# Optimization experiments

Hardware: AMD Instinct MI355X
Metric: run time of the kernel (lower is better)

## Reference

```python
import jax, jax.numpy as jnp
import numpy as np
import math

N, Tp1, V = 256, 33, 10000
D_FEAT, H, W_DIM = 1280, 512, 256
NULL_IDX = 0


def setup_inputs() -> dict:
    key = jax.random.key(0)
    ks = jax.random.split(key, 10)
    feats = jax.random.normal(ks[0], (N, D_FEAT, 4, 4), dtype=jnp.float32)
    captions = jax.random.randint(ks[1], (N, Tp1), 0, V)
    W_proj = jax.random.normal(ks[2], (D_FEAT, H), dtype=jnp.float32) / math.sqrt(D_FEAT)
    b_proj = jnp.zeros((H,), dtype=jnp.float32)
    W_embed = jax.random.normal(ks[3], (V, W_DIM), dtype=jnp.float32) / math.sqrt(V)
    Wx = jax.random.normal(ks[4], (W_DIM, 4 * H), dtype=jnp.float32) / math.sqrt(W_DIM)
    Wh = jax.random.normal(ks[5], (H, 4 * H), dtype=jnp.float32) / math.sqrt(H)
    Wattn = jax.random.normal(ks[6], (H, 4 * H), dtype=jnp.float32) / math.sqrt(H)
    b = jnp.zeros((4 * H,), dtype=jnp.float32)
    W_vocab = jax.random.normal(ks[7], (H, V), dtype=jnp.float32) / math.sqrt(H)
    b_vocab = jnp.zeros((V,), dtype=jnp.float32)
    return {"feats": feats, "captions": captions, "W_proj": W_proj, "b_proj": b_proj,
            "W_embed": W_embed, "Wx": Wx, "Wh": Wh, "Wattn": Wattn, "b": b,
            "W_vocab": W_vocab, "b_vocab": b_vocab}


def _attention_lstm(x, A_flat, h0, Wx, Wh, Wattn, b):
    # x: (N,T,W), A_flat: (N,H,16), h0: (N,H)
    Hh = h0.shape[1]
    scale = 1.0 / math.sqrt(Hh)

    def step(carry, x_t):
        h, c = carry
        # scaled dot-product attention over the 16 spatial positions
        scores = jnp.einsum('nh,nhp->np', h, A_flat) * scale       # (N,16)
        w = jax.nn.softmax(scores, axis=1)
        attn = jnp.einsum('nhp,np->nh', A_flat, w)                 # (N,H)
        a = x_t @ Wx + h @ Wh + b + attn @ Wattn                   # (N,4H)
        i = jax.nn.sigmoid(a[:, 0:Hh])
        f = jax.nn.sigmoid(a[:, Hh:2 * Hh])
        o = jax.nn.sigmoid(a[:, 2 * Hh:3 * Hh])
        g = jnp.tanh(a[:, 3 * Hh:4 * Hh])
        c_next = f * c + i * g
        h_next = o * jnp.tanh(c_next)
        return (h_next, c_next), h_next

    (_, _), hs = jax.lax.scan(step, (h0, h0), jnp.swapaxes(x, 0, 1))
    return jnp.swapaxes(hs, 0, 1)  # (N,T,H)


def reference(feats, captions, W_proj, b_proj, W_embed, Wx, Wh, Wattn, b, W_vocab, b_vocab):
    cap_in = captions[:, :-1]   # (N,T)
    cap_out = captions[:, 1:]   # (N,T)
    # project CNN features per spatial location: (N,Dfeat,4,4) -> (N,H,4,4)
    A = jnp.einsum('ncij,ch->nhij', feats, W_proj) + b_proj[None, :, None, None]
    h0 = A.mean(axis=(2, 3))                     # (N,H); c0 = h0
    A_flat = A.reshape(A.shape[0], A.shape[1], 16)
    x = W_embed[cap_in]                           # (N,T,W)
    h = _attention_lstm(x, A_flat, h0, Wx, Wh, Wattn, b)
    scores = jnp.einsum('nth,hv->ntv', h, W_vocab) + b_vocab   # (N,T,V)
    # temporal softmax loss, sum over tokens (ignoring NULL), averaged over N
    logp = jax.nn.log_softmax(scores, axis=-1)
    nll = -jnp.take_along_axis(logp, cap_out[..., None], axis=-1)[..., 0]  # (N,T)
    mask = (cap_out != NULL_IDX).astype(scores.dtype)
    loss = jnp.sum(nll * mask) / scores.shape[0]
    return loss
```

## Files before the change

### kernel.cpp

```cpp
#include <hip/hip_runtime.h>
#include <hip/hip_bf16.h>

#define NB   256
#define NT   32
#define NV   10000
#define NVP  10240
#define NDF  1280
#define NH   512
#define VT_N 40

typedef short bf16x8 __attribute__((ext_vector_type(8)));
typedef float f32x4  __attribute__((ext_vector_type(4)));
typedef unsigned short u16;

__device__ __forceinline__ float b2f(u16 u) {
    union { unsigned i; float f; } v; v.i = ((unsigned)u) << 16; return v.f;
}
__device__ __forceinline__ u16 f2b(float f) {
    union { float f; unsigned i; } v; v.f = f;
    unsigned r = v.i + 0x7FFF + ((v.i >> 16) & 1);
    return (u16)(r >> 16);
}

__device__ __forceinline__ void gload16(const u16* g, u16* l) {
    __builtin_amdgcn_global_load_lds(
        (const __attribute__((address_space(1))) void*)g,
        (__attribute__((address_space(3))) void*)l, 16, 0, 0);
}

static const size_t B_C     = 0;
static const size_t B_SCP   = B_C     + (size_t)256*512*4;
static const size_t B_PMAX  = B_SCP   + (size_t)2*32*256*16*4;
static const size_t B_PSUM  = B_PMAX  + (size_t)8192*VT_N*4;
static const size_t B_TGT   = B_PSUM  + (size_t)8192*VT_N*4;
static const size_t B_LOSS  = B_TGT   + (size_t)8192*4;
static const size_t B_AB    = B_LOSS  + 16;
static const size_t B_XPB   = B_AB    + (size_t)256*16*512*2;
static const size_t B_HALLB = B_XPB   + (size_t)32*256*2048*2;
static const size_t B_WVT   = B_HALLB + (size_t)32*256*512*2;
static const size_t B_WXT   = B_WVT   + (size_t)10240*512*2;
static const size_t B_WHAT  = B_WXT   + (size_t)2048*256*2;
static const size_t B_HB0   = B_WHAT  + (size_t)2048*1024*2;
static const size_t B_HB1   = B_HB0   + (size_t)256*512*2;
static const size_t B_PREAW = B_HB1   + (size_t)256*512*2;

__global__ __launch_bounds__(256) void tconv_kernel(
    const float* __restrict__ src, u16* __restrict__ dst,
    int K, int N, int Npad, int ldK, int koff)
{
    __shared__ u16 tile[64][65];
    const int k0 = blockIdx.y * 64, n0 = blockIdx.x * 64, tid = threadIdx.x;
#pragma unroll
    for (int i = 0; i < 16; i++) {
        int idx = tid + i * 256;
        int kk = idx >> 6, nn = idx & 63;
        int n = n0 + nn;
        float v = (n < N) ? src[(size_t)(k0 + kk) * N + n] : 0.f;
        tile[kk][nn] = f2b(v);
    }
    __syncthreads();
#pragma unroll
    for (int i = 0; i < 16; i++) {
        int idx = tid + i * 256;
        int nn = idx >> 6, kk = idx & 63;
        int n = n0 + nn;
        if (n < Npad) dst[(size_t)n * ldK + koff + k0 + kk] = tile[kk][nn];
    }
}

__global__ __launch_bounds__(256) void ftrans_kernel(
    const float* __restrict__ feats, u16* __restrict__ fT)
{
    const int cch = blockIdx.x, n = blockIdx.y, tid = threadIdx.x;
    __shared__ u16 lt[64][17];
    const int c0 = cch * 64;
    const int c = tid >> 2, p4 = (tid & 3) * 4;
    float4 v = *(const float4*)(feats + (size_t)n * 20480 + (size_t)(c0 + c) * 16 + p4);
    lt[c][p4] = f2b(v.x); lt[c][p4 + 1] = f2b(v.y);
    lt[c][p4 + 2] = f2b(v.z); lt[c][p4 + 3] = f2b(v.w);
    __syncthreads();
    const int p = tid >> 4, cg = tid & 15;
    ushort4 o;
    o.x = lt[cg * 4 + 0][p]; o.y = lt[cg * 4 + 1][p];
    o.z = lt[cg * 4 + 2][p]; o.w = lt[cg * 4 + 3][p];
    *(ushort4*)(fT + (size_t)(n * 16 + p) * 1280 + c0 + cg * 4) = o;
}

__global__ __launch_bounds__(256) void proj_gemm_kernel(
    const u16* __restrict__ fT, const u16* __restrict__ WpT,
    const float* __restrict__ bp, u16* __restrict__ Ab)
{
    const int ct = blockIdx.x, rt = blockIdx.y;
    const int tid = threadIdx.x, w = tid >> 6, lane = tid & 63;
    const int r0 = rt * 64;
    const int lm = lane & 15, lkq = lane >> 4, lk = lkq * 8;
    const int nbase = ct * 128 + w * 32;

    f32x4 acc[4][2];
#pragma unroll
    for (int mt = 0; mt < 4; mt++)
#pragma unroll
        for (int nt = 0; nt < 2; nt++) acc[mt][nt] = (f32x4){0.f, 0.f, 0.f, 0.f};

    for (int kc = 0; kc < 1280; kc += 32) {
        bf16x8 af[4];
#pragma unroll
        for (int mt = 0; mt < 4; mt++)
            af[mt] = *(const bf16x8*)(fT + (size_t)(r0 + mt * 16 + lm) * 1280 + kc + lk);
#pragma unroll
        for (int nt = 0; nt < 2; nt++) {
            bf16x8 bfg = *(const bf16x8*)(WpT + (size_t)(nbase + nt * 16 + lm) * 1280 + kc + lk);
#pragma unroll
            for (int mt = 0; mt < 4; mt++)
                acc[mt][nt] = __builtin_amdgcn_mfma_f32_16x16x32_bf16(af[mt], bfg, acc[mt][nt], 0, 0, 0);
        }
    }
    float bbv[2];
#pragma unroll
    for (int nt = 0; nt < 2; nt++) bbv[nt] = bp[nbase + nt * 16 + lm];
#pragma unroll
    for (int mt = 0; mt < 4; mt++)
#pragma unroll
        for (int nt = 0; nt < 2; nt++)
#pragma unroll
            for (int r = 0; r < 4; r++) {
                int row = r0 + mt * 16 + lkq * 4 + r;
                int col = nbase + nt * 16 + lm;
                Ab[(size_t)row * 512 + col] = f2b(acc[mt][nt][r] + bbv[nt]);
            }
}

__global__ __launch_bounds__(256) void projmean_kernel(
    const u16* __restrict__ Ab, float* __restrict__ c0, u16* __restrict__ hb0)
{
    const int n = blockIdx.x, tid = threadIdx.x;
    const int col0 = tid, col1 = tid + 256;
    float s0 = 0.f, s1 = 0.f;
#pragma unroll
    for (int p = 0; p < 16; p++) {
        const u16* ap = Ab + ((size_t)n * 16 + p) * 512;
        s0 += b2f(ap[col0]);
        s1 += b2f(ap[col1]);
    }
    s0 *= 0.0625f; s1 *= 0.0625f;
    c0[n * 512 + col0] = s0;  c0[n * 512 + col1] = s1;
    hb0[(size_t)n * 512 + col0] = f2b(s0);
    hb0[(size_t)n * 512 + col1] = f2b(s1);
}

__global__ __launch_bounds__(256) void xp_mfma_kernel(
    const int* __restrict__ caps, const float* __restrict__ We,
    const u16* __restrict__ Wxt, const float* __restrict__ bb,
    u16* __restrict__ xpb)
{
    const int ct = blockIdx.x, rt = blockIdx.y;
    const int tid = threadIdx.x, w = tid >> 6, lane = tid & 63;
    const int r0 = rt * 64;
    const int lm = lane & 15, lkq = lane >> 4, lk = lkq * 8;
    const int nbase = ct * 512 + w * 128;

    int capm[4];
#pragma unroll
    for (int mt = 0; mt < 4; mt++) {
        int row = r0 + mt * 16 + lm;
        capm[mt] = caps[(row >> 5) * 33 + (row & 31)];
    }
    f32x4 acc[4][8];
#pragma unroll
    for (int mt = 0; mt < 4; mt++)
#pragma unroll
        for (int nt = 0; nt < 8; nt++) acc[mt][nt] = (f32x4){0.f, 0.f, 0.f, 0.f};

    for (int kc = 0; kc < 256; kc += 32) {
        bf16x8 af[4];
#pragma unroll
        for (int mt = 0; mt < 4; mt++) {
            const float* ap = We + (size_t)capm[mt] * 256 + kc + lk;
            float4 f0 = *(const float4*)ap;
            float4 f1 = *(const float4*)(ap + 4);
            bf16x8 t;
            t[0] = (short)f2b(f0.x); t[1] = (short)f2b(f0.y);
            t[2] = (short)f2b(f0.z); t[3] = (short)f2b(f0.w);
            t[4] = (short)f2b(f1.x); t[5] = (short)f2b(f1.y);
            t[6] = (short)f2b(f1.z); t[7] = (short)f2b(f1.w);
            af[mt] = t;
        }
#pragma unroll
        for (int nt = 0; nt < 8; nt++) {
            bf16x8 bfg = *(const bf16x8*)(Wxt + (size_t)(nbase + nt * 16 + lm) * 256 + kc + lk);
#pragma unroll
            for (int mt = 0; mt < 4; mt++)
                acc[mt][nt] = __builtin_amdgcn_mfma_f32_16x16x32_bf16(af[mt], bfg, acc[mt][nt], 0, 0, 0);
        }
    }
    float bbv[8];
#pragma unroll
    for (int nt = 0; nt < 8; nt++) bbv[nt] = bb[nbase + nt * 16 + lm];
#pragma unroll
    for (int mt = 0; mt < 4; mt++)
#pragma unroll
        for (int nt = 0; nt < 8; nt++)
#pragma unroll
            for (int r = 0; r < 4; r++) {
                int row = r0 + mt * 16 + lkq * 4 + r;
                int col = nbase + nt * 16 + lm;
                float v = acc[mt][nt][r] + bbv[nt];
                xpb[((size_t)(row & 31) * 256 + (row >> 5)) * 2048 + col] = f2b(v);
            }
}

__global__ __launch_bounds__(256) void preaw_mfma_kernel(
    const u16* __restrict__ Ab, const u16* __restrict__ what,
    u16* __restrict__ preaw)
{
    const int ct = blockIdx.x, rt = blockIdx.y;
    const int tid = threadIdx.x, w = tid >> 6, lane = tid & 63;
    const int r0 = rt * 64;
    const int lm = lane & 15, lkq = lane >> 4, lk = lkq * 8;
    const int nbase = ct * 512 + w * 128;

    f32x4 acc[4][8];
#pragma unroll
    for (int mt = 0; mt < 4; mt++)
#pragma unroll
        for (int nt = 0; nt < 8; nt++) acc[mt][nt] = (f32x4){0.f, 0.f, 0.f, 0.f};

    for (int kc = 0; kc < 512; kc += 32) {
        bf16x8 af[4];
#pragma unroll
        for (int mt = 0; mt < 4; mt++)
            af[mt] = *(const bf16x8*)(Ab + (size_t)(r0 + mt * 16 + lm) * 512 + kc + lk);
#pragma unroll
        for (int nt = 0; nt < 8; nt++) {
            bf16x8 bfg = *(const bf16x8*)(what + (size_t)(nbase + nt * 16 + lm) * 1024 + 512 + kc + lk);
#pragma unroll
            for (int mt = 0; mt < 4; mt++)
                acc[mt][nt] = __builtin_amdgcn_mfma_f32_16x16x32_bf16(af[mt], bfg, acc[mt][nt], 0, 0, 0);
        }
    }
#pragma unroll
    for (int mt = 0; mt < 4; mt++) {
        int nIdx = (r0 >> 4) + mt;
#pragma unroll
        for (int nt = 0; nt < 8; nt++) {
            int col = nbase + nt * 16 + lm;
            ushort4 o;
            o.x = f2b(acc[mt][nt][0]); o.y = f2b(acc[mt][nt][1]);
            o.z = f2b(acc[mt][nt][2]); o.w = f2b(acc[mt][nt][3]);
            *(ushort4*)(preaw + (size_t)nIdx * 32768 + (size_t)col * 16 + lkq * 4) = o;
        }
    }
}

__global__ __launch_bounds__(64) void score_init_kernel(
    const u16* __restrict__ hb0, const u16* __restrict__ Ab,
    float* __restrict__ scp)
{
    const int n = blockIdx.x, lane = threadIdx.x;
    const u16* hp = hb0 + (size_t)n * 512 + lane * 8;
    ushort4 h0 = *(const ushort4*)hp, h1 = *(const ushort4*)(hp + 4);
    float hv0 = b2f(h0.x), hv1 = b2f(h0.y), hv2 = b2f(h0.z), hv3 = b2f(h0.w);
    float hv4 = b2f(h1.x), hv5 = b2f(h1.y), hv6 = b2f(h1.z), hv7 = b2f(h1.w);
    float mine = 0.f;
#pragma unroll
    for (int p = 0; p < 16; p++) {
        const u16* ap = Ab + (size_t)n * 8192 + p * 512 + lane * 8;
        ushort4 a0 = *(const ushort4*)ap, a1 = *(const ushort4*)(ap + 4);
        float s = hv0*b2f(a0.x) + hv1*b2f(a0.y) + hv2*b2f(a0.z) + hv3*b2f(a0.w)
                + hv4*b2f(a1.x) + hv5*b2f(a1.y) + hv6*b2f(a1.z) + hv7*b2f(a1.w);
#pragma unroll
        for (int mask = 1; mask <= 32; mask <<= 1) s += __shfl_xor(s, mask, 64);
        if (lane == p) mine = s;
    }
    if (lane < 16) scp[n * 16 + lane] = mine;
    for (int i = lane; i < 31 * 16; i += 64)
        scp[(1 + (i >> 4)) * 4096 + n * 16 + (i & 15)] = 0.f;
}

__global__ __launch_bounds__(256, 2) void gates_fused_kernel(
    const u16* __restrict__ hb_in, const float* __restrict__ scp_in,
    const u16* __restrict__ what, const u16* __restrict__ preaw,
    const u16* __restrict__ xpt, const u16* __restrict__ Ab,
    float* __restrict__ c, u16* __restrict__ hb_out,
    u16* __restrict__ hallbt, float* __restrict__ scp_out)
{
    const int rt = blockIdx.x, cg = blockIdx.y;
    const int tid = threadIdx.x, ty = tid >> 6, lane = tid & 63;
    const int lm = lane & 15, lkq = lane >> 4, lk = lkq * 8;
    const int r0 = rt * 16, hc0 = cg * 16;

    __shared__ u16 hs[16 * 520];
    __shared__ float sred[16][17];
    __shared__ float wts[16][17];
    __shared__ float gred[4][16][18];
    __shared__ u16 hnew[16][16];

    const int col = ty * 512 + hc0 + lm;

    const u16* brow = what + (size_t)col * 1024 + lk;
    bf16x8 bfa[16];
#pragma unroll
    for (int i = 0; i < 16; i++) bfa[i] = *(const bf16x8*)(brow + i * 32);

    ushort4 pwv[4][4];
#pragma unroll
    for (int r = 0; r < 4; r++) {
        const u16* pp = preaw + (size_t)(r0 + lkq * 4 + r) * 32768 + (size_t)col * 16;
#pragma unroll
        for (int j = 0; j < 4; j++) pwv[r][j] = *(const ushort4*)(pp + j * 4);
    }
    u16 xpw[4];
#pragma unroll
    for (int r = 0; r < 4; r++) xpw[r] = xpt[(size_t)(r0 + lkq * 4 + r) * 2048 + col];

    const int rg = lkq * 4 + ty;
    const int idxg = (r0 + rg) * 512 + hc0 + lm;
    float cin = c[idxg];

    const int rs = tid >> 4, ps = tid & 15;
    ushort4 abv[4];
    {
        const u16* ap = Ab + (size_t)(r0 + rs) * 8192 + ps * 512 + hc0;
#pragma unroll
        for (int j = 0; j < 4; j++) abv[j] = *(const ushort4*)(ap + j * 4);
    }

#pragma unroll
    for (int i = 0; i < 8; i++) {
        int fid = tid + i * 256;
        int rr = fid >> 7, c4 = fid & 127;
        *(ushort4*)&hs[rr * 520 + c4 * 4] =
            *(const ushort4*)(hb_in + (size_t)(r0 + rr) * 512 + c4 * 4);
    }
    {
        float s = 0.f;
#pragma unroll
        for (int g = 0; g < 32; g++) s += scp_in[g * 4096 + (r0 + rs) * 16 + ps];
        sred[rs][ps] = s * 0.04419417382415922f;
    }
    __syncthreads();
    {
        float m = -1e30f;
#pragma unroll
        for (int q = 0; q < 16; q++) m = fmaxf(m, sred[rs][q]);
        float su = 0.f;
#pragma unroll
        for (int q = 0; q < 16; q++) su += __expf(sred[rs][q] - m);
        wts[rs][ps] = __expf(sred[rs][ps] - m) / su;
    }
    f32x4 acc = (f32x4){0.f, 0.f, 0.f, 0.f};
    const u16* arow = &hs[lm * 520 + lk];
#pragma unroll
    for (int i = 0; i < 16; i++) {
        bf16x8 af = *(const bf16x8*)(arow + i * 32);
        acc = __builtin_amdgcn_mfma_f32_16x16x32_bf16(af, bfa[i], acc, 0, 0, 0);
    }
    __syncthreads();
#pragma unroll
    for (int r = 0; r < 4; r++) {
        const int rl = lkq * 4 + r;
        float s = acc[r] + b2f(xpw[r]);
#pragma unroll
        for (int j = 0; j < 4; j++) {
            s += wts[rl][j * 4 + 0] * b2f(pwv[r][j].x);
            s += wts[rl][j * 4 + 1] * b2f(pwv[r][j].y);
            s += wts[rl][j * 4 + 2] * b2f(pwv[r][j].z);
            s += wts[rl][j * 4 + 3] * b2f(pwv[r][j].w);
        }
        gred[ty][rl][lm] = s;
    }
    __syncthreads();
    {
        float ai  = gred[0][rg][lm];
        float af_ = gred[1][rg][lm];
        float ao  = gred[2][rg][lm];
        float ag  = gred[3][rg][lm];
        float ig = 1.f / (1.f + __expf(-ai));
        float fg = 1.f / (1.f + __expf(-af_));
        float og = 1.f / (1.f + __expf(-ao));
        float gv = tanhf(ag);
        float cn = fg * cin + ig * gv;
        float hn = og * tanhf(cn);
        c[idxg] = cn;
        u16 hbv = f2b(hn);
        hb_out[idxg] = hbv;
        hallbt[idxg] = hbv;
        hnew[rg][lm] = hbv;
    }
    __syncthreads();
    {
        float s = 0.f;
#pragma unroll
        for (int j = 0; j < 4; j++) {
            s += b2f(hnew[rs][j * 4 + 0]) * b2f(abv[j].x);
            s += b2f(hnew[rs][j * 4 + 1]) * b2f(abv[j].y);
            s += b2f(hnew[rs][j * 4 + 2]) * b2f(abv[j].z);
            s += b2f(hnew[rs][j * 4 + 3]) * b2f(abv[j].w);
        }
        scp_out[cg * 4096 + (r0 + rs) * 16 + ps] = s;
    }
}

__global__ __launch_bounds__(512) void vocab_mfma_kernel(
    const u16* __restrict__ hallb, const u16* __restrict__ Wvt,
    const float* __restrict__ bv, const int* __restrict__ caps,
    float* __restrict__ pmax, float* __restrict__ psum, float* __restrict__ tgt)
{
    const int ct = blockIdx.x, rt = blockIdx.y;
    const int tid = threadIdx.x, w = tid >> 6, lane = tid & 63;
    const int wr = w >> 2, wc = w & 3;
    const int r0 = rt * 128, c0 = ct * 256;
    const int lm = lane & 15, lkq = lane >> 4;
    const int swz = lkq ^ ((lm >> 1) & 3);

    __shared__ u16 As[2][512 * 8];
    __shared__ u16 Bs[2][1024 * 8];
    __shared__ int tvs[128];
    __shared__ float cm[128][4], cs[128][4];

    if (tid < 128) {
        int row = r0 + tid;
        tvs[tid] = caps[(row & 255) * 33 + (row >> 8) + 1];
    }

    f32x4 acc[4][4];
#pragma unroll
    for (int mt = 0; mt < 4; mt++)
#pragma unroll
        for (int nt = 0; nt < 4; nt++) acc[mt][nt] = (f32x4){0.f, 0.f, 0.f, 0.f};

    const int sA = w * 64 + lane;
    const int rA = sA >> 2, kA = (sA & 3) ^ ((rA >> 1) & 3);
    const u16* gA = hallb + (size_t)(r0 + rA) * 512 + kA * 8;
    const int sB0 = w * 64 + lane, sB1 = sB0 + 512;
    const int cB0 = sB0 >> 2, kB0 = (sB0 & 3) ^ ((cB0 >> 1) & 3);
    const int cB1 = sB1 >> 2, kB1 = (sB1 & 3) ^ ((cB1 >> 1) & 3);
    const u16* gB0 = Wvt + (size_t)(c0 + cB0) * 512 + kB0 * 8;
    const u16* gB1 = Wvt + (size_t)(c0 + cB1) * 512 + kB1 * 8;

    auto stage = [&](int buf, int kc) {
        gload16(gA + kc, &As[buf][w * 512]);
        gload16(gB0 + kc, &Bs[buf][w * 512]);
        gload16(gB1 + kc, &Bs[buf][(w + 8) * 512]);
    };
    auto compute = [&](int buf) {
        bf16x8 af[4], bfr[4];
#pragma unroll
        for (int mt = 0; mt < 4; mt++)
            af[mt] = *(const bf16x8*)&As[buf][((wr * 64 + mt * 16 + lm) * 4 + swz) * 8];
#pragma unroll
        for (int nt = 0; nt < 4; nt++)
            bfr[nt] = *(const bf16x8*)&Bs[buf][((wc * 64 + nt * 16 + lm) * 4 + swz) * 8];
#pragma unroll
        for (int nt = 0; nt < 4; nt++)
#pragma unroll
            for (int mt = 0; mt < 4; mt++)
                acc[mt][nt] = __builtin_amdgcn_mfma_f32_16x16x32_bf16(af[mt], bfr[nt], acc[mt][nt], 0, 0, 0);
    };

    stage(0, 0);
#pragma unroll 1
    for (int t = 0; t < 15; ++t) {
        const int cur = t & 1;
        stage(cur ^ 1, (t + 1) * 32);
        asm volatile("s_waitcnt vmcnt(3)" ::: "memory");
        __builtin_amdgcn_s_barrier();
        compute(cur);
        __builtin_amdgcn_s_barrier();
    }
    asm volatile("s_waitcnt vmcnt(0)" ::: "memory");
    __builtin_amdgcn_s_barrier();
    compute(1);

    float bvv[4]; bool vld[4];
#pragma unroll
    for (int nt = 0; nt < 4; nt++) {
        int col = c0 + wc * 64 + nt * 16 + lm;
        vld[nt] = (col < NV);
        bvv[nt] = vld[nt] ? bv[col] : 0.f;
    }
#pragma unroll
    for (int mt = 0; mt < 4; mt++)
#pragma unroll
        for (int r = 0; r < 4; r++) {
            int rloc = wr * 64 + mt * 16 + lkq * 4 + r;
            int row = r0 + rloc;
            int tv = tvs[rloc];
            float vals[4]; float m = -1e30f;
#pragma unroll
            for (int nt = 0; nt < 4; nt++) {
                int col = c0 + wc * 64 + nt * 16 + lm;
                float v = vld[nt] ? (acc[mt][nt][r] + bvv[nt]) : -1e30f;
                vals[nt] = v;
                m = fmaxf(m, v);
                if (col == tv) tgt[row] = v;
            }
#pragma unroll
            for (int mask = 1; mask <= 8; mask <<= 1) m = fmaxf(m, __shfl_xor(m, mask, 64));
            float s = 0.f;
#pragma unroll
            for (int nt = 0; nt < 4; nt++) s += __expf(vals[nt] - m);
#pragma unroll
            for (int mask = 1; mask <= 8; mask <<= 1) s += __shfl_xor(s, mask, 64);
            if (lm == 0) { cm[rloc][wc] = m; cs[rloc][wc] = s; }
        }
    __syncthreads();
    if (tid < 128) {
        float M = -1e30f;
#pragma unroll
        for (int q = 0; q < 4; q++) M = fmaxf(M, cm[tid][q]);
        float S = 0.f;
#pragma unroll
        for (int q = 0; q < 4; q++) S += cs[tid][q] * __expf(cm[tid][q] - M);
        int row = r0 + tid;
        pmax[row * VT_N + ct] = M;
        psum[row * VT_N + ct] = S;
    }
}

__global__ __launch_bounds__(256) void loss_reduce_kernel(
    const float* __restrict__ pmax, const float* __restrict__ psum,
    const float* __restrict__ tgt, const int* __restrict__ caps,
    float* __restrict__ loss)
{
    const int row = blockIdx.x * 256 + threadIdx.x;
    float nll = 0.f;
    const int t = row >> 8, n = row & 255;
    const int tv = caps[n * 33 + t + 1];
    if (tv != 0) {
        float M = -1e30f;
#pragma unroll
        for (int vt = 0; vt < VT_N; vt++) M = fmaxf(M, pmax[row * VT_N + vt]);
        float S = 0.f;
#pragma unroll
        for (int vt = 0; vt < VT_N; vt++) S += psum[row * VT_N + vt] * __expf(pmax[row * VT_N + vt] - M);
        nll = logf(S) + M - tgt[row];
    }
#pragma unroll
    for (int off = 32; off; off >>= 1) nll += __shfl_down(nll, off, 64);
    __shared__ float r4[4];
    if ((threadIdx.x & 63) == 0) r4[threadIdx.x >> 6] = nll;
    __syncthreads();
    if (threadIdx.x == 0)
        atomicAdd(loss, (r4[0] + r4[1] + r4[2] + r4[3]) * (1.f / 256.f));
}

__global__ void finalize_kernel(const float* __restrict__ loss, float* __restrict__ out)
{
    if (threadIdx.x == 0 && blockIdx.x == 0) out[0] = loss[0];
}

extern "C" void kernel_launch(void* const* d_in, const int* in_sizes, int n_in,
                              void* d_out, int out_size, void* d_ws, size_t ws_size,
                              hipStream_t stream) {
    const float* feats = (const float*)d_in[0];
    const int*   caps  = (const int*)d_in[1];
    const float* Wp    = (const float*)d_in[2];
    const float* bp    = (const float*)d_in[3];
    const float* We    = (const float*)d_in[4];
    const float* Wx    = (const float*)d_in[5];
    const float* Wh    = (const float*)d_in[6];
    const float* Wattn = (const float*)d_in[7];
    const float* bb    = (const float*)d_in[8];
    const float* Wv    = (const float*)d_in[9];
    const float* bv    = (const float*)d_in[10];

    char* ws = (char*)d_ws;
    float* c     = (float*)(ws + B_C);
    float* scp0  = (float*)(ws + B_SCP);
    float* scp1  = scp0 + (size_t)32 * 4096;
    float* pmax  = (float*)(ws + B_PMAX);
    float* psum  = (float*)(ws + B_PSUM);
    float* tgt   = (float*)(ws + B_TGT);
    float* loss  = (float*)(ws + B_LOSS);
    u16*   Ab    = (u16*)(ws + B_AB);
    u16*   xpb   = (u16*)(ws + B_XPB);
    u16*   hallb = (u16*)(ws + B_HALLB);
    u16*   wvt   = (u16*)(ws + B_WVT);
    u16*   wxt   = (u16*)(ws + B_WXT);
    u16*   what  = (u16*)(ws + B_WHAT);
    u16*   hb[2] = { (u16*)(ws + B_HB0), (u16*)(ws + B_HB1) };
    u16*   preaw = (u16*)(ws + B_PREAW);
    u16*   fT    = wvt;
    u16*   WpT   = xpb;

    hipMemsetAsync(loss, 0, sizeof(float), stream);

    ftrans_kernel<<<dim3(20, 256), 256, 0, stream>>>(feats, fT);
    tconv_kernel<<<dim3(8, 20), 256, 0, stream>>>(Wp, WpT, 1280, 512, 512, 1280, 0);
    proj_gemm_kernel<<<dim3(4, 64), 256, 0, stream>>>(fT, WpT, bp, Ab);
    projmean_kernel<<<256, 256, 0, stream>>>(Ab, c, hb[0]);

    tconv_kernel<<<dim3(160, 8), 256, 0, stream>>>(Wv, wvt, 512, NV, NVP, 512, 0);
    tconv_kernel<<<dim3(32, 4),  256, 0, stream>>>(Wx, wxt, 256, 2048, 2048, 256, 0);
    tconv_kernel<<<dim3(32, 8),  256, 0, stream>>>(Wh, what, 512, 2048, 2048, 1024, 0);
    tconv_kernel<<<dim3(32, 8),  256, 0, stream>>>(Wattn, what, 512, 2048, 2048, 1024, 512);
    xp_mfma_kernel<<<dim3(4, 128), 256, 0, stream>>>(caps, We, wxt, bb, xpb);
    preaw_mfma_kernel<<<dim3(4, 64), 256, 0, stream>>>(Ab, what, preaw);
    score_init_kernel<<<256, 64, 0, stream>>>(hb[0], Ab, scp0);

    for (int t = 0; t < NT; t++) {
        const int in = t & 1;
        gates_fused_kernel<<<dim3(16, 32), 256, 0, stream>>>(
            hb[in], in ? scp1 : scp0, what, preaw,
            xpb + (size_t)t * 524288, Ab, c,
            hb[1 - in], hallb + (size_t)t * 131072,
            in ? scp0 : scp1);
    }

    vocab_mfma_kernel<<<dim3(VT_N, 64), 512, 0, stream>>>(
        hallb, wvt, bv, caps, pmax, psum, tgt);
    loss_reduce_kernel<<<32, 256, 0, stream>>>(pmax, psum, tgt, caps, loss);
    finalize_kernel<<<1, 64, 0, stream>>>(loss, (float*)d_out);
}
```

Baseline: 744.9 us.

## Replace per-timestep gate launches with one persistent cooperative kernel using grid sync

The 32 per-timestep launches of the fused gates kernel become a single cooperative persistent kernel that loops over timesteps and uses grid.sync between steps. The W_h/W_attn fragments, precomputed attention weights and the cell state stay in registers across all steps instead of being reloaded every launch, and c is no longer written back to global memory. This removes launch overhead and the repeated weight loads. In exchange the 512 blocks must all be co-resident (256 CUs x 2 occupancy), and each grid-wide barrier has its own cost.

```diff
diff --git a/kernel.cpp b/kernel.cpp
--- a/kernel.cpp
+++ b/kernel.cpp
@@ -1,5 +1,8 @@
 #include <hip/hip_runtime.h>
 #include <hip/hip_bf16.h>
+#include <hip/hip_cooperative_groups.h>
+
+namespace cgx = cooperative_groups;
 
 #define NB   256
 #define NT   32
@@ -277,17 +280,18 @@
         scp[(1 + (i >> 4)) * 4096 + n * 16 + (i & 15)] = 0.f;
 }
 
-__global__ __launch_bounds__(256, 2) void gates_fused_kernel(
-    const u16* __restrict__ hb_in, const float* __restrict__ scp_in,
+__global__ __launch_bounds__(256, 2) void gates_persist_kernel(
+    u16* __restrict__ hb0, u16* __restrict__ hb1,
+    float* __restrict__ scp0, float* __restrict__ scp1,
     const u16* __restrict__ what, const u16* __restrict__ preaw,
-    const u16* __restrict__ xpt, const u16* __restrict__ Ab,
-    float* __restrict__ c, u16* __restrict__ hb_out,
-    u16* __restrict__ hallbt, float* __restrict__ scp_out)
-{
-    const int rt = blockIdx.x, cg = blockIdx.y;
+    const u16* __restrict__ xpb, const u16* __restrict__ Ab,
+    const float* __restrict__ cst, u16* __restrict__ hallb)
+{
+    cgx::grid_group grid = cgx::this_grid();
+    const int rt = blockIdx.x, cgi = blockIdx.y;
     const int tid = threadIdx.x, ty = tid >> 6, lane = tid & 63;
     const int lm = lane & 15, lkq = lane >> 4, lk = lkq * 8;
-    const int r0 = rt * 16, hc0 = cg * 16;
+    const int r0 = rt * 16, hc0 = cgi * 16;
 
     __shared__ u16 hs[16 * 520];
     __shared__ float sred[16][17];
@@ -309,13 +313,9 @@
 #pragma unroll
         for (int j = 0; j < 4; j++) pwv[r][j] = *(const ushort4*)(pp + j * 4);
     }
-    u16 xpw[4];
-#pragma unroll
-    for (int r = 0; r < 4; r++) xpw[r] = xpt[(size_t)(r0 + lkq * 4 + r) * 2048 + col];
-
     const int rg = lkq * 4 + ty;
     const int idxg = (r0 + rg) * 512 + hc0 + lm;
-    float cin = c[idxg];
+    float cin = cst[idxg];
 
     const int rs = tid >> 4, ps = tid & 15;
     ushort4 abv[4];
@@ -325,79 +325,95 @@
         for (int j = 0; j < 4; j++) abv[j] = *(const ushort4*)(ap + j * 4);
     }
 
-#pragma unroll
-    for (int i = 0; i < 8; i++) {
-        int fid = tid + i * 256;
-        int rr = fid >> 7, c4 = fid & 127;
-        *(ushort4*)&hs[rr * 520 + c4 * 4] =
-            *(const ushort4*)(hb_in + (size_t)(r0 + rr) * 512 + c4 * 4);
-    }
-    {
-        float s = 0.f;
-#pragma unroll
-        for (int g = 0; g < 32; g++) s += scp_in[g * 4096 + (r0 + rs) * 16 + ps];
-        sred[rs][ps] = s * 0.04419417382415922f;
-    }
-    __syncthreads();
-    {
-        float m = -1e30f;
-#pragma unroll
-        for (int q = 0; q < 16; q++) m = fmaxf(m, sred[rs][q]);
-        float su = 0.f;
-#pragma unroll
-        for (int q = 0; q < 16; q++) su += __expf(sred[rs][q] - m);
-        wts[rs][ps] = __expf(sred[rs][ps] - m) / su;
-    }
-    f32x4 acc = (f32x4){0.f, 0.f, 0.f, 0.f};
-    const u16* arow = &hs[lm * 520 + lk];
-#pragma unroll
-    for (int i = 0; i < 16; i++) {
-        bf16x8 af = *(const bf16x8*)(arow + i * 32);
-        acc = __builtin_amdgcn_mfma_f32_16x16x32_bf16(af, bfa[i], acc, 0, 0, 0);
-    }
-    __syncthreads();
-#pragma unroll
-    for (int r = 0; r < 4; r++) {
-        const int rl = lkq * 4 + r;
-        float s = acc[r] + b2f(xpw[r]);
-#pragma unroll
-        for (int j = 0; j < 4; j++) {
-            s += wts[rl][j * 4 + 0] * b2f(pwv[r][j].x);
-            s += wts[rl][j * 4 + 1] * b2f(pwv[r][j].y);
-            s += wts[rl][j * 4 + 2] * b2f(pwv[r][j].z);
-            s += wts[rl][j * 4 + 3] * b2f(pwv[r][j].w);
-        }
-        gred[ty][rl][lm] = s;
-    }
-    __syncthreads();
-    {
-        float ai  = gred[0][rg][lm];
-        float af_ = gred[1][rg][lm];
-        float ao  = gred[2][rg][lm];
-        float ag  = gred[3][rg][lm];
-        float ig = 1.f / (1.f + __expf(-ai));
-        float fg = 1.f / (1.f + __expf(-af_));
-        float og = 1.f / (1.f + __expf(-ao));
-        float gv = tanhf(ag);
-        float cn = fg * cin + ig * gv;
-        float hn = og * tanhf(cn);
-        c[idxg] = cn;
-        u16 hbv = f2b(hn);
-        hb_out[idxg] = hbv;
-        hallbt[idxg] = hbv;
-        hnew[rg][lm] = hbv;
-    }
-    __syncthreads();
-    {
-        float s = 0.f;
-#pragma unroll
-        for (int j = 0; j < 4; j++) {
-            s += b2f(hnew[rs][j * 4 + 0]) * b2f(abv[j].x);
-            s += b2f(hnew[rs][j * 4 + 1]) * b2f(abv[j].y);
-            s += b2f(hnew[rs][j * 4 + 2]) * b2f(abv[j].z);
-            s += b2f(hnew[rs][j * 4 + 3]) * b2f(abv[j].w);
-        }
-        scp_out[cg * 4096 + (r0 + rs) * 16 + ps] = s;
+#pragma unroll 1
+    for (int t = 0; t < NT; ++t) {
+        const u16* hbi = (t & 1) ? hb1 : hb0;
+        u16* hbo = (t & 1) ? hb0 : hb1;
+        const float* sin_ = (t & 1) ? scp1 : scp0;
+        float* sout = (t & 1) ? scp0 : scp1;
+        u16* hout = hallb + (size_t)t * 131072;
+        const u16* xpt = xpb + (size_t)t * 524288;
+
+        u16 xpw[4];
+#pragma unroll
+        for (int r = 0; r < 4; r++)
+            xpw[r] = xpt[(size_t)(r0 + lkq * 4 + r) * 2048 + col];
+
+#pragma unroll
+        for (int i = 0; i < 8; i++) {
+            int fid = tid + i * 256;
+            int rr = fid >> 7, c4 = fid & 127;
+            *(ushort4*)&hs[rr * 520 + c4 * 4] =
+                *(const ushort4*)(hbi + (size_t)(r0 + rr) * 512 + c4 * 4);
+        }
+        {
+            float s = 0.f;
+#pragma unroll
+            for (int g = 0; g < 32; g++) s += sin_[g * 4096 + (r0 + rs) * 16 + ps];
+            sred[rs][ps] = s * 0.04419417382415922f;
+        }
+        __syncthreads();
+        {
+            float m = -1e30f;
+#pragma unroll
+            for (int q = 0; q < 16; q++) m = fmaxf(m, sred[rs][q]);
+            float su = 0.f;
+#pragma unroll
+            for (int q = 0; q < 16; q++) su += __expf(sred[rs][q] - m);
+            wts[rs][ps] = __expf(sred[rs][ps] - m) / su;
+        }
+        f32x4 acc = (f32x4){0.f, 0.f, 0.f, 0.f};
+        const u16* arow = &hs[lm * 520 + lk];
+#pragma unroll
+        for (int i = 0; i < 16; i++) {
+            bf16x8 af = *(const bf16x8*)(arow + i * 32);
+            acc = __builtin_amdgcn_mfma_f32_16x16x32_bf16(af, bfa[i], acc, 0, 0, 0);
+        }
+        __syncthreads();
+#pragma unroll
+        for (int r = 0; r < 4; r++) {
+            const int rl = lkq * 4 + r;
+            float s = acc[r] + b2f(xpw[r]);
+#pragma unroll
+            for (int j = 0; j < 4; j++) {
+                s += wts[rl][j * 4 + 0] * b2f(pwv[r][j].x);
+                s += wts[rl][j * 4 + 1] * b2f(pwv[r][j].y);
+                s += wts[rl][j * 4 + 2] * b2f(pwv[r][j].z);
+                s += wts[rl][j * 4 + 3] * b2f(pwv[r][j].w);
+            }
+            gred[ty][rl][lm] = s;
+        }
+        __syncthreads();
+        {
+            float ai  = gred[0][rg][lm];
+            float af_ = gred[1][rg][lm];
+            float ao  = gred[2][rg][lm];
+            float ag  = gred[3][rg][lm];
+            float ig = 1.f / (1.f + __expf(-ai));
+            float fg = 1.f / (1.f + __expf(-af_));
+            float og = 1.f / (1.f + __expf(-ao));
+            float gv = tanhf(ag);
+            float cn = fg * cin + ig * gv;
+            float hn = og * tanhf(cn);
+            cin = cn;
+            u16 hbv = f2b(hn);
+            hbo[idxg] = hbv;
+            hout[idxg] = hbv;
+            hnew[rg][lm] = hbv;
+        }
+        __syncthreads();
+        {
+            float s = 0.f;
+#pragma unroll
+            for (int j = 0; j < 4; j++) {
+                s += b2f(hnew[rs][j * 4 + 0]) * b2f(abv[j].x);
+                s += b2f(hnew[rs][j * 4 + 1]) * b2f(abv[j].y);
+                s += b2f(hnew[rs][j * 4 + 2]) * b2f(abv[j].z);
+                s += b2f(hnew[rs][j * 4 + 3]) * b2f(abv[j].w);
+            }
+            sout[cgi * 4096 + (r0 + rs) * 16 + ps] = s;
+        }
+        if (t != NT - 1) grid.sync();
     }
 }
 
@@ -599,13 +615,16 @@
     preaw_mfma_kernel<<<dim3(4, 64), 256, 0, stream>>>(Ab, what, preaw);
     score_init_kernel<<<256, 64, 0, stream>>>(hb[0], Ab, scp0);
 
-    for (int t = 0; t < NT; t++) {
-        const int in = t & 1;
-        gates_fused_kernel<<<dim3(16, 32), 256, 0, stream>>>(
-            hb[in], in ? scp1 : scp0, what, preaw,
-            xpb + (size_t)t * 524288, Ab, c,
-            hb[1 - in], hallb + (size_t)t * 131072,
-            in ? scp0 : scp1);
+    {
+        u16* hb0p = hb[0]; u16* hb1p = hb[1];
+        float* s0p = scp0; float* s1p = scp1;
+        const u16* whatp = what; const u16* preawp = preaw;
+        const u16* xpbp = xpb; const u16* Abp = Ab;
+        const float* cp = c; u16* hallbp = hallb;
+        void* kargs[] = { &hb0p, &hb1p, &s0p, &s1p,
+                          &whatp, &preawp, &xpbp, &Abp, &cp, &hallbp };
+        hipLaunchCooperativeKernel((const void*)gates_persist_kernel,
+                                   dim3(16, 32), dim3(256), kargs, 0, stream);
     }
 
     vocab_mfma_kernel<<<dim3(VT_N, 64), 512, 0, stream>>>(
```

After: 2.622 ms. +252.0%, slower.
